# Kernel tuning notes

Hardware: AMD Instinct MI355X
Metric: run time of the kernel (lower is better)

## Reference

```python
import jax, jax.numpy as jnp
import numpy as np

B, S, D = 2, 2048, 1024
H = 4096          # expert FFN hidden
E = 8             # num experts
K = 2             # top-k
RH = 256          # router GRU hidden


def setup_inputs() -> dict:
    key = jax.random.key(0)
    ks = jax.random.split(key, 10)
    std = 0.02
    return {
        "hidden_states": jax.random.normal(ks[0], (B, S, D), jnp.float32),
        # stacked expert weights (torch Linear weight layout: (out, in))
        "Wg": jax.random.normal(ks[1], (E, H, D), jnp.float32) * std,  # gate_proj
        "Wu": jax.random.normal(ks[2], (E, H, D), jnp.float32) * std,  # up_proj
        "Wd": jax.random.normal(ks[3], (E, D, H), jnp.float32) * std,  # down_proj
        # GRU router params (torch GRUCell layout)
        "W_ih": jax.random.normal(ks[4], (3 * RH, D), jnp.float32) * std,
        "W_hh": jax.random.normal(ks[5], (3 * RH, RH), jnp.float32) * std,
        "b_ih": jnp.zeros((3 * RH,), jnp.float32),
        "b_hh": jnp.zeros((3 * RH,), jnp.float32),
        # router output projection to expert logits
        "Wr": jax.random.normal(ks[6], (E, RH), jnp.float32) * std,
        "br": jnp.zeros((E,), jnp.float32),
    }


def _gru_router(x, W_ih, W_hh, b_ih, b_hh, Wr, br):
    """GRUCell over sequence. x: (B,S,D) -> logits (B,S,E), last hidden (B,RH)."""
    # precompute input-side gates for all steps: (B,S,3RH)
    gi_all = jnp.einsum('bsd,gd->bsg', x, W_ih) + b_ih

    def step(h, gi_t):  # h: (B,RH), gi_t: (B,3RH)
        gh = h @ W_hh.T + b_hh
        i_r, i_z, i_n = jnp.split(gi_t, 3, axis=-1)
        h_r, h_z, h_n = jnp.split(gh, 3, axis=-1)
        r = jax.nn.sigmoid(i_r + h_r)
        z = jax.nn.sigmoid(i_z + h_z)
        n = jnp.tanh(i_n + r * h_n)
        h_new = (1.0 - z) * n + z * h
        return h_new, h_new

    h0 = jnp.zeros((x.shape[0], RH), x.dtype)
    last_h, hs = jax.lax.scan(step, h0, jnp.swapaxes(gi_all, 0, 1))  # hs: (S,B,RH)
    hs = jnp.swapaxes(hs, 0, 1)  # (B,S,RH)
    logits = jnp.einsum('bsr,er->bse', hs, Wr) + br
    return logits, last_h


def reference(hidden_states, Wg, Wu, Wd, W_ih, W_hh, b_ih, b_hh, Wr, br):
    x = hidden_states
    router_logits, new_hidden = _gru_router(x, W_ih, W_hh, b_ih, b_hh, Wr, br)
    router_probs = jax.nn.softmax(router_logits, axis=-1)  # (B,S,E)

    # load-balancing aux loss (probs-based)
    mean_probs = router_probs.mean(axis=(0, 1))  # (E,)
    aux_loss = E * jnp.sum(mean_probs * mean_probs)

    # top-k gating, renormalized
    topk_p, topk_idx = jax.lax.top_k(router_probs, K)  # (B,S,K)
    topk_p = topk_p / topk_p.sum(axis=-1, keepdims=True)
    # dense per-expert gate weights (B,S,E); zeros for non-selected experts
    w_dense = jnp.sum(jax.nn.one_hot(topk_idx, E, dtype=x.dtype) * topk_p[..., None], axis=2)

    # dense-masked expert compute (same math: zero-weight experts contribute 0)
    out = jnp.zeros((B, S, D), x.dtype)
    for e in range(E):
        h = jax.nn.gelu(jnp.einsum('bsd,hd->bsh', x, Wg[e]), approximate=False) \
            * jnp.einsum('bsd,hd->bsh', x, Wu[e])
        out = out + jnp.einsum('bsh,dh->bsd', h, Wd[e]) * w_dense[..., e:e + 1]

    return out, router_logits, new_hidden, aux_loss
```

## Files before the change

### kernel.cpp

```cpp
#include <hip/hip_runtime.h>
#include <cstdint>
#include <cstddef>

#define B_  2
#define S_  2048
#define D_  1024
#define HH_ 4096
#define E_  8
#define RH_ 256

typedef float  f32x4 __attribute__((ext_vector_type(4)));
typedef float  f32x2 __attribute__((ext_vector_type(2)));
typedef __bf16 bf16x8 __attribute__((ext_vector_type(8)));
typedef __bf16 bf16x4 __attribute__((ext_vector_type(4)));

__device__ __forceinline__ void gload_lds16(const void* g, void* l) {
  __builtin_amdgcn_global_load_lds(
      (const __attribute__((address_space(1))) unsigned int*)g,
      (__attribute__((address_space(3))) unsigned int*)l, 16, 0, 0);
}

__device__ __forceinline__ void stage128x64(__bf16* s, const __bf16* g, int ldK, int t) {
  const int wv = t >> 6, l = t & 63;
#pragma unroll
  for (int p = 0; p < 4; ++p) {
    const int base = p * 256 + wv * 64;
    const int flat = base + l;
    const int row = flat >> 3, c16 = flat & 7;
    gload_lds16(g + (size_t)row * ldK + c16 * 8, s + (size_t)base * 8);
  }
}

__device__ __forceinline__ void stage128x64_cvt(__bf16* s, const float* g, int ldK, int t) {
#pragma unroll
  for (int p = 0; p < 4; ++p) {
    const int flat = p * 256 + t;
    const int row = flat >> 3, c8 = (flat & 7) << 3;
    const float* src = g + (size_t)row * ldK + c8;
    f32x4 a = *(const f32x4*)src;
    f32x4 b = *(const f32x4*)(src + 4);
    bf16x8 o;
#pragma unroll
    for (int j2 = 0; j2 < 4; ++j2) { o[j2] = (__bf16)a[j2]; o[4 + j2] = (__bf16)b[j2]; }
    *(bf16x8*)&s[(size_t)flat * 8] = o;
  }
}

__device__ __forceinline__ void stage128x64_gather(__bf16* s, const __bf16* src,
                                                   int ldK, int k0,
                                                   const int* rowtok, int t) {
  const int wv = t >> 6, l = t & 63;
#pragma unroll
  for (int p = 0; p < 4; ++p) {
    const int base = p * 256 + wv * 64;
    const int flat = base + l;
    const int row = flat >> 3, c16 = flat & 7;
    const int tok = rowtok[row];
    gload_lds16(src + (size_t)tok * ldK + k0 + c16 * 8, s + (size_t)base * 8);
  }
}

__device__ __forceinline__ void mfma_tile(const __bf16* sA, const __bf16* sB,
                                          f32x4 acc[4][4], int t) {
  const int w = t >> 6, l = t & 63;
  const int wr = w >> 1, wc = w & 1;
  const int fr = l & 15, fk = (l >> 4) * 8;
#pragma unroll
  for (int kk = 0; kk < 2; ++kk) {
    bf16x8 a[4], b[4];
#pragma unroll
    for (int m = 0; m < 4; ++m)
      a[m] = *(const bf16x8*)&sA[(64 * wr + 16 * m + fr) * 64 + kk * 32 + fk];
#pragma unroll
    for (int n = 0; n < 4; ++n)
      b[n] = *(const bf16x8*)&sB[(64 * wc + 16 * n + fr) * 64 + kk * 32 + fk];
#pragma unroll
    for (int m = 0; m < 4; ++m)
#pragma unroll
      for (int n = 0; n < 4; ++n)
        acc[m][n] = __builtin_amdgcn_mfma_f32_16x16x32_bf16(a[m], b[n], acc[m][n], 0, 0, 0);
  }
}

__device__ __forceinline__ void mfma_tile2(const __bf16* sA, const __bf16* sB,
                                           const __bf16* sC, f32x4 accg[4][4],
                                           f32x4 accu[4][4], int t) {
  const int w = t >> 6, l = t & 63;
  const int wr = w >> 1, wc = w & 1;
  const int fr = l & 15, fk = (l >> 4) * 8;
#pragma unroll
  for (int kk = 0; kk < 2; ++kk) {
    bf16x8 a[4], bg[4], bu[4];
#pragma unroll
    for (int m = 0; m < 4; ++m)
      a[m] = *(const bf16x8*)&sA[(64 * wr + 16 * m + fr) * 64 + kk * 32 + fk];
#pragma unroll
    for (int n = 0; n < 4; ++n) {
      bg[n] = *(const bf16x8*)&sB[(64 * wc + 16 * n + fr) * 64 + kk * 32 + fk];
      bu[n] = *(const bf16x8*)&sC[(64 * wc + 16 * n + fr) * 64 + kk * 32 + fk];
    }
#pragma unroll
    for (int m = 0; m < 4; ++m)
#pragma unroll
      for (int n = 0; n < 4; ++n) {
        accg[m][n] = __builtin_amdgcn_mfma_f32_16x16x32_bf16(a[m], bg[n], accg[m][n], 0, 0, 0);
        accu[m][n] = __builtin_amdgcn_mfma_f32_16x16x32_bf16(a[m], bu[n], accu[m][n], 0, 0, 0);
      }
  }
}

__device__ __forceinline__ f32x2 pkfma(f32x2 a, f32x2 b, f32x2 d) {
  asm("v_pk_fma_f32 %0, %1, %2, %0" : "+v"(d) : "v"(a), "v"(b));
  return d;
}

__device__ __forceinline__ float fexp(float x) {
  return __builtin_amdgcn_exp2f(x * 1.44269504088896f);
}
__device__ __forceinline__ float fsig(float x) {
  return __builtin_amdgcn_rcpf(1.f + fexp(-x));
}
__device__ __forceinline__ float ftanh(float x) {
  return 1.f - 2.f * __builtin_amdgcn_rcpf(fexp(2.f * x) + 1.f);
}

__global__ void k_split3(const float* __restrict__ src, __bf16* __restrict__ hi,
                         __bf16* __restrict__ mid, __bf16* __restrict__ lo, int n4) {
  int i = blockIdx.x * 256 + threadIdx.x;
  if (i >= n4) return;
  f32x4 v = ((const f32x4*)src)[i];
  bf16x4 h, m, l;
#pragma unroll
  for (int j = 0; j < 4; ++j) {
    float x = v[j];
    __bf16 hb = (__bf16)x;
    float r1 = x - (float)hb;
    __bf16 mb = (__bf16)r1;
    float r2 = r1 - (float)mb;
    h[j] = hb; m[j] = mb; l[j] = (__bf16)r2;
  }
  ((bf16x4*)hi)[i] = h; ((bf16x4*)mid)[i] = m; ((bf16x4*)lo)[i] = l;
}

__global__ void k_cvt1(const float* __restrict__ src, __bf16* __restrict__ dst, int n4) {
  int i = blockIdx.x * 256 + threadIdx.x;
  if (i >= n4) return;
  f32x4 v = ((const f32x4*)src)[i];
  bf16x4 o;
#pragma unroll
  for (int j = 0; j < 4; ++j) o[j] = (__bf16)v[j];
  ((bf16x4*)dst)[i] = o;
}

__global__ __launch_bounds__(256, 2)
void k_gemm_gi(const __bf16* __restrict__ xh, const __bf16* __restrict__ xm,
               const __bf16* __restrict__ xl, const __bf16* __restrict__ wh,
               const __bf16* __restrict__ wm, const __bf16* __restrict__ wl,
               const float* __restrict__ bih, float* __restrict__ gi) {
  __shared__ __bf16 sA[128 * 64], sB[128 * 64];
  const int t = threadIdx.x;
  const int m0 = blockIdx.x * 128, n0 = blockIdx.y * 128;
  f32x4 acc[4][4] = {};
  const __bf16* As[6] = {xh, xh, xm, xh, xm, xl};
  const __bf16* Bs[6] = {wh, wm, wh, wl, wm, wh};
  for (int p = 0; p < 6; ++p) {
    const __bf16* A = As[p];
    const __bf16* Bm = Bs[p];
    for (int kt = 0; kt < D_ / 64; ++kt) {
      __syncthreads();
      stage128x64(sA, A + (size_t)m0 * D_ + kt * 64, D_, t);
      stage128x64(sB, Bm + (size_t)n0 * D_ + kt * 64, D_, t);
      __syncthreads();
      mfma_tile(sA, sB, acc, t);
    }
  }
  const int w = t >> 6, l = t & 63, wr = w >> 1, wc = w & 1;
  const int col = l & 15, rb = (l >> 4) * 4;
#pragma unroll
  for (int m = 0; m < 4; ++m)
#pragma unroll
    for (int n = 0; n < 4; ++n)
#pragma unroll
      for (int i = 0; i < 4; ++i) {
        int gm = m0 + 64 * wr + 16 * m + rb + i;
        int gn = n0 + 64 * wc + 16 * n + col;
        gi[(size_t)gm * 768 + gn] = acc[m][n][i] + bih[gn];
      }
}

__global__ __attribute__((amdgpu_flat_work_group_size(512, 512)))
__attribute__((amdgpu_waves_per_eu(2, 2)))
void k_fused(const float* __restrict__ Whh, const float* __restrict__ gi,
             const float* __restrict__ bhh, float* __restrict__ hs,
             float* __restrict__ newh,
             const __bf16* __restrict__ xbf, const float* __restrict__ Wg,
             const float* __restrict__ Wu, __bf16* __restrict__ Hall,
             const float* __restrict__ Wd, __bf16* __restrict__ Wdbf,
             int nGemm) {
  __shared__ __align__(16) char smem[98304];
  const int bid = blockIdx.x;

  if (bid < 16) {
    int role;
    switch (bid) {
      case 0: role = 0; break;
      case 8: role = 1; break;
      case 1: role = 2; break;
      case 9: role = 3; break;
      default: return;
    }
    const int b = role >> 1, half = role & 1;
    const int t = threadIdx.x;
    const int c = t & 3;
    const int q = t >> 2;
    const int g = half * 128 + q;
    float (*hbuf)[256] = (float(*)[256])smem;

    f32x2 w0[32], w1[32], w2[32];
#pragma unroll
    for (int j = 0; j < 16; ++j) {
      const int jr = (j + 2 * c) & 15;
      const size_t colo = (size_t)(64 * c + 4 * jr);
      f32x4 v0 = *(const f32x4*)(Whh + (size_t)g * 256 + colo);
      f32x4 v1 = *(const f32x4*)(Whh + (size_t)(g + 256) * 256 + colo);
      f32x4 v2 = *(const f32x4*)(Whh + (size_t)(g + 512) * 256 + colo);
      w0[2 * j] = f32x2{v0[0], v0[1]}; w0[2 * j + 1] = f32x2{v0[2], v0[3]};
      w1[2 * j] = f32x2{v1[0], v1[1]}; w1[2 * j + 1] = f32x2{v1[2], v1[3]};
      w2[2 * j] = f32x2{v2[0], v2[1]}; w2[2 * j + 1] = f32x2{v2[2], v2[3]};
    }
#pragma unroll
    for (int j = 0; j < 32; ++j) {
      asm("" : "+v"(w0[j]));
      asm("" : "+v"(w1[j]));
      asm("" : "+v"(w2[j]));
    }
    const float bh0 = bhh[g], bh1 = bhh[g + 256], bh2 = bhh[g + 512];
    if (t < 256) hbuf[0][t] = 0.f;
    float h_old = 0.f;
    const float* giB = gi + (size_t)(b * S_) * 768;
    float* hsB = hs + (size_t)b * 256;
    float ir = giB[g], iz = giB[g + 256], in_ = giB[g + 512];
    __syncthreads();

    for (int s = 0; s < S_; ++s) {
      const int cur = s & 1, nxt = cur ^ 1;
      const int sn = (s + 1 < S_) ? s + 1 : s;
      const float irn = giB[(size_t)sn * 768 + g];
      const float izn = giB[(size_t)sn * 768 + g + 256];
      const float inn = giB[(size_t)sn * 768 + g + 512];

      f32x2 a0 = {0.f, 0.f}, a1 = a0, a2 = a0;
#pragma unroll
      for (int j = 0; j < 16; ++j) {
        const int jr = (j + 2 * c) & 15;
        f32x4 hv = *(const f32x4*)&hbuf[cur][64 * c + 4 * jr];
        f32x2 hA = {hv[0], hv[1]}, hB = {hv[2], hv[3]};
        a0 = pkfma(w0[2 * j], hA, a0); a0 = pkfma(w0[2 * j + 1], hB, a0);
        a1 = pkfma(w1[2 * j], hA, a1); a1 = pkfma(w1[2 * j + 1], hB, a1);
        a2 = pkfma(w2[2 * j], hA, a2); a2 = pkfma(w2[2 * j + 1], hB, a2);
      }
      float d0 = (a0[0] + a0[1]);
      float d1 = (a1[0] + a1[1]);
      float d2 = (a2[0] + a2[1]);
      d0 += __shfl_xor(d0, 1); d0 += __shfl_xor(d0, 2);
      d1 += __shfl_xor(d1, 1); d1 += __shfl_xor(d1, 2);
      d2 += __shfl_xor(d2, 1); d2 += __shfl_xor(d2, 2);

      const float r = fsig(ir + d0 + bh0);
      const float z = fsig(iz + d1 + bh1);
      const float n = ftanh(in_ + r * (d2 + bh2));
      const float hn = (1.f - z) * n + z * h_old;
      h_old = hn;

      float* hsrow = hsB + (size_t)s * 512;
      if (c == 0) {
        hbuf[nxt][g] = hn;
        __hip_atomic_store(hsrow + g, hn, __ATOMIC_RELAXED, __HIP_MEMORY_SCOPE_AGENT);
      }
      if (t < 128) {
        const int pg = (half ^ 1) * 128 + t;
        float v;
        do {
          v = __hip_atomic_load(hsrow + pg, __ATOMIC_RELAXED, __HIP_MEMORY_SCOPE_AGENT);
        } while (v != v);
        hbuf[nxt][pg] = v;
      }
      ir = irn; iz = izn; in_ = inn;
      __syncthreads();
    }
    if (c == 0) newh[b * 256 + g] = h_old;

  } else if (bid < 16 + nGemm) {
    const int bi = bid - 16;
    const int e = bi >> 10, r = bi & 1023;
    const int m0 = (r & 31) * 128, n0 = (r >> 5) * 128;
    __bf16* sA = (__bf16*)smem;
    __bf16* sB = sA + 128 * 64;
    __bf16* sC = sB + 128 * 64;
    const int t = threadIdx.x;
    const float* wg = Wg + (size_t)e * HH_ * D_;
    const float* wu = Wu + (size_t)e * HH_ * D_;
    f32x4 ag[4][4] = {}, au[4][4] = {};
    for (int kt = 0; kt < D_ / 64; ++kt) {
      __syncthreads();
      if (t < 256) {
        stage128x64(sA, xbf + (size_t)m0 * D_ + kt * 64, D_, t);
        stage128x64_cvt(sB, wg + (size_t)n0 * D_ + kt * 64, D_, t);
        stage128x64_cvt(sC, wu + (size_t)n0 * D_ + kt * 64, D_, t);
      }
      __syncthreads();
      if (t < 256) mfma_tile2(sA, sB, sC, ag, au, t);
    }
    if (t < 256) {
      const int w = t >> 6, l = t & 63, wr = w >> 1, wc = w & 1;
      const int col = l & 15, rb = (l >> 4) * 4;
#pragma unroll
      for (int m = 0; m < 4; ++m)
#pragma unroll
        for (int n = 0; n < 4; ++n)
#pragma unroll
          for (int i = 0; i < 4; ++i) {
            int gm = m0 + 64 * wr + 16 * m + rb + i;
            int gn = n0 + 64 * wc + 16 * n + col;
            float gv = ag[m][n][i], uv = au[m][n][i];
            float h = 0.5f * gv * (1.f + erff(gv * 0.70710678118654752440f)) * uv;
            Hall[((size_t)e * 4096 + gm) * HH_ + gn] = (__bf16)h;
          }
    }

  } else {
    const int bi2 = bid - 16 - nGemm;
    const size_t base = (size_t)bi2 * 512 + threadIdx.x;
#pragma unroll
    for (int k2 = 0; k2 < 4; ++k2) {
      const size_t u = base + (size_t)k2 * 2097152;
      f32x4 v = ((const f32x4*)Wd)[u];
      bf16x4 o;
#pragma unroll
      for (int j = 0; j < 4; ++j) o[j] = (__bf16)v[j];
      ((bf16x4*)Wdbf)[u] = o;
    }
  }
}

__global__ void k_logits(const float* __restrict__ hs, const float* __restrict__ Wr,
                         const float* __restrict__ br, float* __restrict__ logits) {
  const int idx = blockIdx.x * 256 + threadIdx.x;
  const int tok = idx >> 3, e = idx & 7;
  const int s = tok & (S_ - 1), b = tok >> 11;
  const f32x4* h4 = (const f32x4*)&hs[((size_t)s * 2 + b) * 256];
  const f32x4* w4 = (const f32x4*)&Wr[e * 256];
  float acc = 0.f;
#pragma unroll 8
  for (int k = 0; k < 64; ++k) {
    f32x4 a = h4[k], w = w4[k];
    acc += a[0] * w[0] + a[1] * w[1] + a[2] * w[2] + a[3] * w[3];
  }
  logits[idx] = acc + br[e];
}

__global__ void k_finish(const float* __restrict__ logits, float* __restrict__ wdense,
                         int* __restrict__ idx2, float* __restrict__ partials) {
  const int tok = blockIdx.x * 256 + threadIdx.x;
  float p[8];
  float mx = -1e30f;
#pragma unroll
  for (int e = 0; e < 8; ++e) { p[e] = logits[tok * 8 + e]; mx = fmaxf(mx, p[e]); }
  float sum = 0.f;
#pragma unroll
  for (int e = 0; e < 8; ++e) { p[e] = expf(p[e] - mx); sum += p[e]; }
  const float inv = 1.f / sum;
#pragma unroll
  for (int e = 0; e < 8; ++e) p[e] *= inv;
  int i1 = 0;
#pragma unroll
  for (int e = 1; e < 8; ++e) if (p[e] > p[i1]) i1 = e;
  int i2 = -1; float p2 = -1.f;
#pragma unroll
  for (int e = 0; e < 8; ++e) if (e != i1 && p[e] > p2) { p2 = p[e]; i2 = e; }
  const float inv2 = 1.f / (p[i1] + p2);
#pragma unroll
  for (int e = 0; e < 8; ++e)
    wdense[tok * 8 + e] = (e == i1) ? p[i1] * inv2 : (e == i2 ? p2 * inv2 : 0.f);
  idx2[tok * 2] = i1;
  idx2[tok * 2 + 1] = i2;

  __shared__ float ps[256][8];
#pragma unroll
  for (int e = 0; e < 8; ++e) ps[threadIdx.x][e] = p[e];
  __syncthreads();
  for (int st = 128; st >= 1; st >>= 1) {
    if (threadIdx.x < st)
#pragma unroll
      for (int e = 0; e < 8; ++e) ps[threadIdx.x][e] += ps[threadIdx.x + st][e];
    __syncthreads();
  }
  if (threadIdx.x == 0)
#pragma unroll
    for (int e = 0; e < 8; ++e) partials[blockIdx.x * 8 + e] = ps[0][e];
}

__global__ void k_aux(const float* __restrict__ partials, float* __restrict__ aux) {
  __shared__ float m2[8];
  const int e = threadIdx.x;
  if (e < 8) {
    float s = 0.f;
    for (int bl = 0; bl < 16; ++bl) s += partials[bl * 8 + e];
    const float mean = s / 4096.f;
    m2[e] = mean * mean;
  }
  __syncthreads();
  if (threadIdx.x == 0) {
    float s = 0.f;
#pragma unroll
    for (int i = 0; i < 8; ++i) s += m2[i];
    aux[0] = 8.f * s;
  }
}

__global__ void k_build(const int* __restrict__ idx2, int* __restrict__ cnt,
                        int* __restrict__ list) {
  const int tok = blockIdx.x * 256 + threadIdx.x;
#pragma unroll
  for (int k = 0; k < 2; ++k) {
    const int e = idx2[tok * 2 + k];
    const int pos = atomicAdd(&cnt[e], 1);
    list[e * 4096 + pos] = tok;
  }
}

__global__ __launch_bounds__(256, 2)
void k_gateup_d(const __bf16* __restrict__ xbf, const float* __restrict__ Wg,
                const float* __restrict__ Wu, __bf16* __restrict__ Hout) {
  __shared__ __bf16 sA[128 * 64], sB[128 * 64], sC[128 * 64];
  const int t = threadIdx.x;
  const int m0 = blockIdx.x * 128, n0 = blockIdx.y * 128;
  f32x4 ag[4][4] = {}, au[4][4] = {};
  for (int kt = 0; kt < D_ / 64; ++kt) {
    __syncthreads();
    stage128x64(sA, xbf + (size_t)m0 * D_ + kt * 64, D_, t);
    stage128x64_cvt(sB, Wg + (size_t)n0 * D_ + kt * 64, D_, t);
    stage128x64_cvt(sC, Wu + (size_t)n0 * D_ + kt * 64, D_, t);
    __syncthreads();
    mfma_tile2(sA, sB, sC, ag, au, t);
  }
  const int w = t >> 6, l = t & 63, wr = w >> 1, wc = w & 1;
  const int col = l & 15, rb = (l >> 4) * 4;
#pragma unroll
  for (int m = 0; m < 4; ++m)
#pragma unroll
    for (int n = 0; n < 4; ++n)
#pragma unroll
      for (int i = 0; i < 4; ++i) {
        int gm = m0 + 64 * wr + 16 * m + rb + i;
        int gn = n0 + 64 * wc + 16 * n + col;
        float gv = ag[m][n][i], uv = au[m][n][i];
        float h = 0.5f * gv * (1.f + erff(gv * 0.70710678118654752440f)) * uv;
        Hout[(size_t)gm * HH_ + gn] = (__bf16)h;
      }
}

__global__ __launch_bounds__(256, 2)
void k_down_s(const __bf16* __restrict__ Hbase, const __bf16* __restrict__ Wdbase,
              const float* __restrict__ wdense, const int* __restrict__ list,
              const int* __restrict__ cnt, float* __restrict__ out,
              int eBase, int hRowsPerE, long long wStridePerE) {
  __shared__ __bf16 sA[128 * 64], sB[128 * 64];
  __shared__ int rowtok[128];
  const int e = eBase + blockIdx.z;
  const int t = threadIdx.x;
  const int m0 = blockIdx.x * 128, n0 = blockIdx.y * 128;
  const int ce = cnt[e];
  if (m0 >= ce) return;
  if (t < 128) rowtok[t] = list[e * 4096 + m0 + t];
  const __bf16* Hrows = Hbase + (size_t)e * hRowsPerE * HH_;
  const __bf16* Wde = Wdbase + (size_t)e * (size_t)wStridePerE;
  f32x4 acc[4][4] = {};
  for (int kt = 0; kt < HH_ / 64; ++kt) {
    __syncthreads();
    stage128x64_gather(sA, Hrows, HH_, kt * 64, rowtok, t);
    stage128x64(sB, Wde + (size_t)n0 * HH_ + kt * 64, HH_, t);
    __syncthreads();
    mfma_tile(sA, sB, acc, t);
  }
  const int w = t >> 6, l = t & 63, wr = w >> 1, wc = w & 1;
  const int col = l & 15, rb = (l >> 4) * 4;
#pragma unroll
  for (int m = 0; m < 4; ++m)
#pragma unroll
    for (int i = 0; i < 4; ++i) {
      const int lr = 64 * wr + 16 * m + rb + i;
      if (m0 + lr < ce) {
        const int tok = rowtok[lr];
        const float wv = wdense[tok * 8 + e];
#pragma unroll
        for (int n = 0; n < 4; ++n) {
          const int gn = n0 + 64 * wc + 16 * n + col;
          atomicAdd(&out[(size_t)tok * 1024 + gn], wv * acc[m][n][i]);
        }
      }
    }
}

extern "C" void kernel_launch(void* const* d_in, const int* in_sizes, int n_in,
                              void* d_out, int out_size, void* d_ws, size_t ws_size,
                              hipStream_t stream) {
  (void)in_sizes; (void)n_in; (void)out_size;
  const float* x    = (const float*)d_in[0];
  const float* Wg   = (const float*)d_in[1];
  const float* Wu   = (const float*)d_in[2];
  const float* Wd   = (const float*)d_in[3];
  const float* Wih  = (const float*)d_in[4];
  const float* Whh  = (const float*)d_in[5];
  const float* bih  = (const float*)d_in[6];
  const float* bhh  = (const float*)d_in[7];
  const float* Wr   = (const float*)d_in[8];
  const float* br   = (const float*)d_in[9];

  float* out    = (float*)d_out;
  float* logits = out + (size_t)B_ * S_ * D_;
  float* newh   = logits + (size_t)B_ * S_ * E_;
  float* aux    = newh + (size_t)B_ * RH_;

  char* ws = (char*)d_ws;
  size_t off = 0;
  auto alloc = [&](size_t bytes) { size_t r = off; off += (bytes + 255) & ~(size_t)255; return r; };
  const size_t XN = (size_t)B_ * S_ * D_;
  const size_t WIN = (size_t)3 * RH_ * D_;

  __bf16* xh  = (__bf16*)(ws + alloc(XN * 2));
  __bf16* xm  = (__bf16*)(ws + alloc(XN * 2));
  __bf16* xl  = (__bf16*)(ws + alloc(XN * 2));
  __bf16* wih_h = (__bf16*)(ws + alloc(WIN * 2));
  __bf16* wih_m = (__bf16*)(ws + alloc(WIN * 2));
  __bf16* wih_l = (__bf16*)(ws + alloc(WIN * 2));
  float*  gi  = (float*)(ws + alloc((size_t)B_ * S_ * 768 * 4));
  float*  hs  = (float*)(ws + alloc((size_t)S_ * B_ * RH_ * 4));
  float*  wdense = (float*)(ws + alloc((size_t)B_ * S_ * E_ * 4));
  int*    idx2 = (int*)(ws + alloc((size_t)B_ * S_ * 2 * 4));
  int*    cnt  = (int*)(ws + alloc(E_ * 4));
  int*    list = (int*)(ws + alloc((size_t)E_ * 4096 * 4));
  float*  partials = (float*)(ws + alloc(16 * 8 * 4));
  const size_t commonEnd = off;

  const size_t szWdbfAll = (size_t)E_ * D_ * HH_ * 2;
  const size_t szHall    = (size_t)E_ * 4096 * HH_ * 2;
  const bool fused = (commonEnd + szWdbfAll + szHall + 512) <= ws_size;

  hipMemsetAsync(out, 0, XN * 4, stream);
  hipMemsetAsync(hs, 0xFF, (size_t)S_ * B_ * RH_ * 4, stream);
  hipMemsetAsync(cnt, 0, E_ * 4, stream);
  hipMemsetAsync(list, 0, (size_t)E_ * 4096 * 4, stream);

  k_split3<<<dim3((XN / 4 + 255) / 256), 256, 0, stream>>>(x, xh, xm, xl, (int)(XN / 4));
  k_split3<<<dim3((WIN / 4 + 255) / 256), 256, 0, stream>>>(Wih, wih_h, wih_m, wih_l, (int)(WIN / 4));
  k_gemm_gi<<<dim3(32, 6), 256, 0, stream>>>(xh, xm, xl, wih_h, wih_m, wih_l, bih, gi);

  if (fused) {
    __bf16* WdbfA = (__bf16*)(ws + alloc(szWdbfAll));
    __bf16* Hall  = (__bf16*)(ws + alloc(szHall));
    const int nGemm = E_ * 32 * 32;
    const int nCvt  = 4096;
    k_fused<<<dim3(16 + nGemm + nCvt), 512, 0, stream>>>(
        Whh, gi, bhh, hs, newh, xh, Wg, Wu, Hall, Wd, WdbfA, nGemm);
    k_logits<<<dim3(128), 256, 0, stream>>>(hs, Wr, br, logits);
    k_finish<<<dim3(16), 256, 0, stream>>>(logits, wdense, idx2, partials);
    k_aux<<<dim3(1), 64, 0, stream>>>(partials, aux);
    k_build<<<dim3(16), 256, 0, stream>>>(idx2, cnt, list);
    k_down_s<<<dim3(32, 8, 8), 256, 0, stream>>>(
        Hall, WdbfA, wdense, list, cnt, out, 0, 4096, (long long)D_ * HH_);
  } else {
    __bf16* Wdbf = (__bf16*)(ws + alloc((size_t)D_ * HH_ * 2));
    __bf16* Htmp = (__bf16*)(ws + alloc((size_t)B_ * S_ * HH_ * 2));
    k_fused<<<dim3(16), 512, 0, stream>>>(
        Whh, gi, bhh, hs, newh, xh, Wg, Wu, Htmp, Wd, Wdbf, 0);
    k_logits<<<dim3(128), 256, 0, stream>>>(hs, Wr, br, logits);
    k_finish<<<dim3(16), 256, 0, stream>>>(logits, wdense, idx2, partials);
    k_aux<<<dim3(1), 64, 0, stream>>>(partials, aux);
    k_build<<<dim3(16), 256, 0, stream>>>(idx2, cnt, list);
    const int n4w = (int)((size_t)HH_ * D_ / 4);
    for (int e = 0; e < E_; ++e) {
      const size_t wo = (size_t)e * HH_ * D_;
      k_cvt1<<<dim3((n4w + 255) / 256), 256, 0, stream>>>(Wd + wo, Wdbf, n4w);
      k_gateup_d<<<dim3(32, 32), 256, 0, stream>>>(xh, Wg + wo, Wu + wo, Htmp);
      k_down_s<<<dim3(32, 8, 1), 256, 0, stream>>>(
          Htmp, Wdbf, wdense, list, cnt, out, e, 0, 0);
    }
  }
}
```

Before: 3.306 ms.

## Overlap GRU own-half matvec with peer polling and fuse router kernels

After: 4.495 ms. +35.9%, slower.

```diff
diff --git a/kernel.cpp b/kernel.cpp
--- a/kernel.cpp
+++ b/kernel.cpp
@@ -214,6 +214,9 @@
     const int c = t & 3;
     const int q = t >> 2;
     const int g = half * 128 + q;
+    const bool isOwn = ((c >> 1) == half);
+    const bool isPoller = (c == 2 * (half ^ 1));
+    const int pg = (half ^ 1) * 128 + q;
     float (*hbuf)[256] = (float(*)[256])smem;
 
     f32x2 w0[32], w1[32], w2[32];
@@ -235,11 +238,12 @@
       asm("" : "+v"(w2[j]));
     }
     const float bh0 = bhh[g], bh1 = bhh[g + 256], bh2 = bhh[g + 512];
-    if (t < 256) hbuf[0][t] = 0.f;
+    if (t < 256) { hbuf[0][t] = 0.f; }
     float h_old = 0.f;
     const float* giB = gi + (size_t)(b * S_) * 768;
     float* hsB = hs + (size_t)b * 256;
     float ir = giB[g], iz = giB[g + 256], in_ = giB[g + 512];
+    f32x2 a0 = {0.f, 0.f}, a1 = a0, a2 = a0;
     __syncthreads();
 
     for (int s = 0; s < S_; ++s) {
@@ -249,15 +253,16 @@
       const float izn = giB[(size_t)sn * 768 + g + 256];
       const float inn = giB[(size_t)sn * 768 + g + 512];
 
-      f32x2 a0 = {0.f, 0.f}, a1 = a0, a2 = a0;
-#pragma unroll
-      for (int j = 0; j < 16; ++j) {
-        const int jr = (j + 2 * c) & 15;
-        f32x4 hv = *(const f32x4*)&hbuf[cur][64 * c + 4 * jr];
-        f32x2 hA = {hv[0], hv[1]}, hB = {hv[2], hv[3]};
-        a0 = pkfma(w0[2 * j], hA, a0); a0 = pkfma(w0[2 * j + 1], hB, a0);
-        a1 = pkfma(w1[2 * j], hA, a1); a1 = pkfma(w1[2 * j + 1], hB, a1);
-        a2 = pkfma(w2[2 * j], hA, a2); a2 = pkfma(w2[2 * j + 1], hB, a2);
+      if (!isOwn) {
+#pragma unroll
+        for (int j = 0; j < 16; ++j) {
+          const int jr = (j + 2 * c) & 15;
+          f32x4 hv = *(const f32x4*)&hbuf[cur][64 * c + 4 * jr];
+          f32x2 hA = {hv[0], hv[1]}, hB = {hv[2], hv[3]};
+          a0 = pkfma(w0[2 * j], hA, a0); a0 = pkfma(w0[2 * j + 1], hB, a0);
+          a1 = pkfma(w1[2 * j], hA, a1); a1 = pkfma(w1[2 * j + 1], hB, a1);
+          a2 = pkfma(w2[2 * j], hA, a2); a2 = pkfma(w2[2 * j + 1], hB, a2);
+        }
       }
       float d0 = (a0[0] + a0[1]);
       float d1 = (a1[0] + a1[1]);
@@ -271,24 +276,37 @@
       const float n = ftanh(in_ + r * (d2 + bh2));
       const float hn = (1.f - z) * n + z * h_old;
       h_old = hn;
+      a0 = f32x2{0.f, 0.f}; a1 = a0; a2 = a0;
 
       float* hsrow = hsB + (size_t)s * 512;
       if (c == 0) {
         hbuf[nxt][g] = hn;
         __hip_atomic_store(hsrow + g, hn, __ATOMIC_RELAXED, __HIP_MEMORY_SCOPE_AGENT);
-      }
-      if (t < 128) {
-        const int pg = (half ^ 1) * 128 + t;
+        if (s == S_ - 1) newh[b * 256 + g] = hn;
+      }
+      __syncthreads();
+
+      if (isPoller) {
         float v;
         do {
           v = __hip_atomic_load(hsrow + pg, __ATOMIC_RELAXED, __HIP_MEMORY_SCOPE_AGENT);
         } while (v != v);
         hbuf[nxt][pg] = v;
       }
+      if (isOwn) {
+#pragma unroll
+        for (int j = 0; j < 16; ++j) {
+          const int jr = (j + 2 * c) & 15;
+          f32x4 hv = *(const f32x4*)&hbuf[nxt][64 * c + 4 * jr];
+          f32x2 hA = {hv[0], hv[1]}, hB = {hv[2], hv[3]};
+          a0 = pkfma(w0[2 * j], hA, a0); a0 = pkfma(w0[2 * j + 1], hB, a0);
+          a1 = pkfma(w1[2 * j], hA, a1); a1 = pkfma(w1[2 * j + 1], hB, a1);
+          a2 = pkfma(w2[2 * j], hA, a2); a2 = pkfma(w2[2 * j + 1], hB, a2);
+        }
+      }
       ir = irn; iz = izn; in_ = inn;
       __syncthreads();
     }
-    if (c == 0) newh[b * 256 + g] = h_old;
 
   } else if (bid < 16 + nGemm) {
     const int bi = bid - 16;
@@ -343,29 +361,29 @@
   }
 }
 
-__global__ void k_logits(const float* __restrict__ hs, const float* __restrict__ Wr,
-                         const float* __restrict__ br, float* __restrict__ logits) {
-  const int idx = blockIdx.x * 256 + threadIdx.x;
-  const int tok = idx >> 3, e = idx & 7;
+__global__ void k_router(const float* __restrict__ hs, const float* __restrict__ Wr,
+                         const float* __restrict__ br, float* __restrict__ logits,
+                         float* __restrict__ wdense, int* __restrict__ cnt,
+                         int* __restrict__ list, float* __restrict__ partials) {
+  const int tok = blockIdx.x * 256 + threadIdx.x;
   const int s = tok & (S_ - 1), b = tok >> 11;
   const f32x4* h4 = (const f32x4*)&hs[((size_t)s * 2 + b) * 256];
-  const f32x4* w4 = (const f32x4*)&Wr[e * 256];
-  float acc = 0.f;
-#pragma unroll 8
-  for (int k = 0; k < 64; ++k) {
-    f32x4 a = h4[k], w = w4[k];
-    acc += a[0] * w[0] + a[1] * w[1] + a[2] * w[2] + a[3] * w[3];
-  }
-  logits[idx] = acc + br[e];
-}
-
-__global__ void k_finish(const float* __restrict__ logits, float* __restrict__ wdense,
-                         int* __restrict__ idx2, float* __restrict__ partials) {
-  const int tok = blockIdx.x * 256 + threadIdx.x;
   float p[8];
   float mx = -1e30f;
 #pragma unroll
-  for (int e = 0; e < 8; ++e) { p[e] = logits[tok * 8 + e]; mx = fmaxf(mx, p[e]); }
+  for (int e = 0; e < 8; ++e) {
+    const f32x4* w4 = (const f32x4*)&Wr[e * 256];
+    float acc = 0.f;
+#pragma unroll 8
+    for (int k = 0; k < 64; ++k) {
+      f32x4 a = h4[k], w = w4[k];
+      acc += a[0] * w[0] + a[1] * w[1] + a[2] * w[2] + a[3] * w[3];
+    }
+    acc += br[e];
+    logits[tok * 8 + e] = acc;
+    p[e] = acc;
+    mx = fmaxf(mx, acc);
+  }
   float sum = 0.f;
 #pragma unroll
   for (int e = 0; e < 8; ++e) { p[e] = expf(p[e] - mx); sum += p[e]; }
@@ -382,8 +400,12 @@
 #pragma unroll
   for (int e = 0; e < 8; ++e)
     wdense[tok * 8 + e] = (e == i1) ? p[i1] * inv2 : (e == i2 ? p2 * inv2 : 0.f);
-  idx2[tok * 2] = i1;
-  idx2[tok * 2 + 1] = i2;
+  {
+    int pos = atomicAdd(&cnt[i1], 1);
+    list[i1 * 4096 + pos] = tok;
+    pos = atomicAdd(&cnt[i2], 1);
+    list[i2 * 4096 + pos] = tok;
+  }
 
   __shared__ float ps[256][8];
 #pragma unroll
@@ -415,17 +437,6 @@
 #pragma unroll
     for (int i = 0; i < 8; ++i) s += m2[i];
     aux[0] = 8.f * s;
-  }
-}
-
-__global__ void k_build(const int* __restrict__ idx2, int* __restrict__ cnt,
-                        int* __restrict__ list) {
-  const int tok = blockIdx.x * 256 + threadIdx.x;
-#pragma unroll
-  for (int k = 0; k < 2; ++k) {
-    const int e = idx2[tok * 2 + k];
-    const int pos = atomicAdd(&cnt[e], 1);
-    list[e * 4096 + pos] = tok;
   }
 }
 
@@ -537,7 +548,6 @@
   float*  gi  = (float*)(ws + alloc((size_t)B_ * S_ * 768 * 4));
   float*  hs  = (float*)(ws + alloc((size_t)S_ * B_ * RH_ * 4));
   float*  wdense = (float*)(ws + alloc((size_t)B_ * S_ * E_ * 4));
-  int*    idx2 = (int*)(ws + alloc((size_t)B_ * S_ * 2 * 4));
   int*    cnt  = (int*)(ws + alloc(E_ * 4));
   int*    list = (int*)(ws + alloc((size_t)E_ * 4096 * 4));
   float*  partials = (float*)(ws + alloc(16 * 8 * 4));
@@ -563,10 +573,8 @@
     const int nCvt  = 4096;
     k_fused<<<dim3(16 + nGemm + nCvt), 512, 0, stream>>>(
         Whh, gi, bhh, hs, newh, xh, Wg, Wu, Hall, Wd, WdbfA, nGemm);
-    k_logits<<<dim3(128), 256, 0, stream>>>(hs, Wr, br, logits);
-    k_finish<<<dim3(16), 256, 0, stream>>>(logits, wdense, idx2, partials);
+    k_router<<<dim3(16), 256, 0, stream>>>(hs, Wr, br, logits, wdense, cnt, list, partials);
     k_aux<<<dim3(1), 64, 0, stream>>>(partials, aux);
-    k_build<<<dim3(16), 256, 0, stream>>>(idx2, cnt, list);
     k_down_s<<<dim3(32, 8, 8), 256, 0, stream>>>(
         Hall, WdbfA, wdense, list, cnt, out, 0, 4096, (long long)D_ * HH_);
   } else {
@@ -574,10 +582,8 @@
     __bf16* Htmp = (__bf16*)(ws + alloc((size_t)B_ * S_ * HH_ * 2));
     k_fused<<<dim3(16), 512, 0, stream>>>(
         Whh, gi, bhh, hs, newh, xh, Wg, Wu, Htmp, Wd, Wdbf, 0);
-    k_logits<<<dim3(128), 256, 0, stream>>>(hs, Wr, br, logits);
-    k_finish<<<dim3(16), 256, 0, stream>>>(logits, wdense, idx2, partials);
+    k_router<<<dim3(16), 256, 0, stream>>>(hs, Wr, br, logits, wdense, cnt, list, partials);
     k_aux<<<dim3(1), 64, 0, stream>>>(partials, aux);
-    k_build<<<dim3(16), 256, 0, stream>>>(idx2, cnt, list);
     const int n4w = (int)((size_t)HH_ * D_ / 4);
     for (int e = 0; e < E_; ++e) {
       const size_t wo = (size_t)e * HH_ * D_;
```
